# Performance work log

Hardware: AMD Instinct MI355X
Metric: run time of the kernel (lower is better)

Reference implementation:

```python
import jax, jax.numpy as jnp
import numpy as np

B, C, L = 8, 256, 2048


def setup_inputs() -> dict:
    key = jax.random.key(0)
    ks = jax.random.split(key, 7)
    s = 0.05
    return {
        "x": jax.random.normal(ks[0], (B, C, L), dtype=jnp.float32),
        "Wq": jax.random.normal(ks[1], (C, C), dtype=jnp.float32) * s,
        "bq": jax.random.normal(ks[2], (C,), dtype=jnp.float32) * s,
        "Wk": jax.random.normal(ks[3], (C, C), dtype=jnp.float32) * s,
        "bk": jax.random.normal(ks[4], (C,), dtype=jnp.float32) * s,
        "Wv": jax.random.normal(ks[5], (C, C), dtype=jnp.float32) * s,
        "bv": jax.random.normal(ks[6], (C,), dtype=jnp.float32) * s,
    }


def reference(x, Wq, bq, Wk, bk, Wv, bv):
    # Conv1d with kernel_size=1 == per-position linear over channels.
    # x: [B, C, L]
    scale = x.shape[1] ** (-0.5)
    q = jnp.einsum('oc,bcl->bol', Wq, x) + bq[None, :, None]  # [B,C,L]
    k = jnp.einsum('oc,bcl->bol', Wk, x) + bk[None, :, None]
    v = jnp.einsum('oc,bcl->bol', Wv, x) + bv[None, :, None]
    scores = jnp.einsum('bcl,bcm->blm', q, k) * scale          # [B,L,L]
    attn = jax.nn.softmax(scores, axis=-1)
    context = jnp.einsum('blm,bcm->bcl', attn, v)              # [B,C,L]
    return context + x
```

## Files before the change

### kernel.cpp

```cpp
#include <hip/hip_runtime.h>

#define NB 8
#define NC 256
#define NL 2048
#define SCALE 0.0625f

typedef __attribute__((ext_vector_type(8))) __bf16 bf16x8;
typedef __attribute__((ext_vector_type(4))) float f32x4;
typedef __attribute__((ext_vector_type(4))) unsigned int u32x4;
typedef __attribute__((ext_vector_type(2))) unsigned int u32x2;
typedef __attribute__((ext_vector_type(4))) unsigned short u16x4;
typedef __attribute__((ext_vector_type(8))) unsigned short u16x8;

static __device__ __forceinline__ unsigned short f2b(float f) {
    unsigned int u = __builtin_bit_cast(unsigned int, f);
    u += 0x7fffu + ((u >> 16) & 1u);
    return (unsigned short)(u >> 16);
}

__global__ void wconv_kernel(const float* __restrict__ Wq,
                             const float* __restrict__ Wk,
                             const float* __restrict__ Wv,
                             unsigned short* __restrict__ Wbf)
{
    const int base = (blockIdx.x * 256 + threadIdx.x) * 4;
    const int mat  = base >> 16;
    const int off  = base & 65535;
    const float* W = (mat == 0) ? Wq : (mat == 1) ? Wk : Wv;
    float4 w = *(const float4*)&W[off];
    u16x4 p = {f2b(w.x), f2b(w.y), f2b(w.z), f2b(w.w)};
    *(u16x4*)&Wbf[base] = p;
}

__global__ __launch_bounds__(256, 2) void xprep_kernel(
    const float* __restrict__ x, unsigned short* __restrict__ xT)
{
    const int b  = blockIdx.z;
    const int c0 = blockIdx.y * 64;
    const int l0 = blockIdx.x * 64;
    const int t  = threadIdx.x;

    __shared__ unsigned short Tr[64][68];

    #pragma unroll
    for (int p = 0; p < 4; ++p) {
        const int c  = p * 16 + (t >> 4);
        const int lg = t & 15;
        float4 xv = *(const float4*)&x[((size_t)(b * NC + c0 + c)) * NL + l0 + lg * 4];
        u16x4 pk = {f2b(xv.x), f2b(xv.y), f2b(xv.z), f2b(xv.w)};
        *(u16x4*)&Tr[c][lg * 4] = pk;
    }
    __syncthreads();
    #pragma unroll
    for (int j = 0; j < 2; ++j) {
        const int chunk = t + 256 * j;
        const int l  = chunk >> 3;
        const int ck = chunk & 7;
        u16x8 o;
        #pragma unroll
        for (int i = 0; i < 8; ++i) o[i] = Tr[ck * 8 + i][l];
        *(u16x8*)&xT[((size_t)(b * NL + l0 + l)) * NC + c0 + ck * 8] = o;
    }
}

__global__ __launch_bounds__(256, 2) void qkv_mfma(
    const unsigned short* __restrict__ xT,
    const unsigned short* __restrict__ Wbf,
    const float* __restrict__ bq, const float* __restrict__ bk,
    const float* __restrict__ bv,
    unsigned short* __restrict__ qT, unsigned short* __restrict__ kT,
    unsigned short* __restrict__ vo)
{
    const int raw = blockIdx.x;
    const int b   = raw & 7;
    const int rem = raw >> 3;
    const int mat = rem >> 5;
    const int lt0 = (rem & 31) * 64;
    const int t    = threadIdx.x;
    const int w    = t >> 6;
    const int lane = t & 63;
    const int ln15 = lane & 15;
    const int quad = lane >> 4;

    __shared__ __align__(16) unsigned short XT[64 * 256];
    __shared__ __align__(16) unsigned short WC[256 * 64];

    const unsigned short* Wm = Wbf + mat * 65536;
    const float* bias = (mat == 0) ? bq : (mat == 1) ? bk : bv;

    float bvals[4][4];
    #pragma unroll
    for (int ot = 0; ot < 4; ++ot)
        #pragma unroll
        for (int r = 0; r < 4; ++r)
            bvals[ot][r] = bias[w * 64 + ot * 16 + quad * 4 + r];

    #pragma unroll
    for (int s = 0; s < 8; ++s) {
        const int il = w * 8 + s;
        const int n  = il * 2 + (lane >> 5);
        const int p  = lane & 31;
        const int g  = p ^ (n & 15);
        const unsigned short* gp = &xT[((size_t)(b * NL + lt0 + n)) * NC + g * 8];
        __builtin_amdgcn_global_load_lds(
            (const __attribute__((address_space(1))) unsigned int*)gp,
            (__attribute__((address_space(3))) unsigned int*)&XT[il * 512],
            16, 0, 0);
    }

    f32x4 acc[4][4];
    #pragma unroll
    for (int i = 0; i < 4; ++i)
        #pragma unroll
        for (int j = 0; j < 4; ++j) acc[i][j] = f32x4{0.f, 0.f, 0.f, 0.f};

    for (int k0 = 0; k0 < 4; ++k0) {
        if (k0) __syncthreads();
        #pragma unroll
        for (int s = 0; s < 8; ++s) {
            const int il = w * 8 + s;
            const int o  = il * 8 + (lane >> 3);
            const int p  = lane & 7;
            const int g  = p ^ (o & 7);
            const unsigned short* gp = &Wm[(size_t)o * NC + k0 * 64 + g * 8];
            __builtin_amdgcn_global_load_lds(
                (const __attribute__((address_space(1))) unsigned int*)gp,
                (__attribute__((address_space(3))) unsigned int*)&WC[il * 512],
                16, 0, 0);
        }
        __syncthreads();

        #pragma unroll
        for (int ks = 0; ks < 2; ++ks) {
            bf16x8 xf[4];
            #pragma unroll
            for (int lt = 0; lt < 4; ++lt) {
                const int l  = lt * 16 + ln15;
                const int kc = k0 * 8 + ks * 4 + quad;
                const int pp = kc ^ (l & 15);
                xf[lt] = __builtin_bit_cast(bf16x8, *(const u32x4*)&XT[l * 256 + pp * 8]);
            }
            #pragma unroll
            for (int ot = 0; ot < 4; ++ot) {
                const int o  = w * 64 + ot * 16 + ln15;
                const int pp = (ks * 4 + quad) ^ (o & 7);
                bf16x8 wf = __builtin_bit_cast(bf16x8, *(const u32x4*)&WC[o * 64 + pp * 8]);
                #pragma unroll
                for (int lt = 0; lt < 4; ++lt)
                    acc[ot][lt] = __builtin_amdgcn_mfma_f32_16x16x32_bf16(
                                      wf, xf[lt], acc[ot][lt], 0, 0, 0);
            }
        }
    }

    if (mat < 2) {
        unsigned short* out = (mat == 0) ? qT : kT;
        #pragma unroll
        for (int ot = 0; ot < 4; ++ot) {
            const int o_base = w * 64 + ot * 16 + quad * 4;
            #pragma unroll
            for (int lt = 0; lt < 4; ++lt) {
                const int l = lt0 + lt * 16 + ln15;
                u16x4 pk;
                #pragma unroll
                for (int r = 0; r < 4; ++r)
                    pk[r] = f2b(acc[ot][lt][r] + bvals[ot][r]);
                *(u16x4*)&out[((size_t)(b * NL + l)) * NC + o_base] = pk;
            }
        }
    } else {
        #pragma unroll
        for (int ot = 0; ot < 4; ++ot)
            #pragma unroll
            for (int lt = 0; lt < 4; ++lt) {
                const int l = lt0 + lt * 16 + ln15;
                #pragma unroll
                for (int r = 0; r < 4; ++r) {
                    const int o = w * 64 + ot * 16 + quad * 4 + r;
                    vo[((size_t)(b * NC + o)) * NL + l] = f2b(acc[ot][lt][r] + bvals[ot][r]);
                }
            }
    }
}

__global__ __launch_bounds__(1024, 4) void attn_kernel(
    const unsigned short* __restrict__ qT,
    const unsigned short* __restrict__ kT,
    const unsigned short* __restrict__ v,
    const float* __restrict__ x,
    float* __restrict__ out)
{
    const int raw  = blockIdx.x;
    const int b    = raw & 7;
    const int l0   = (raw >> 3) * 64;
    const int t    = threadIdx.x;
    const int w    = t >> 6;
    const int lane = t & 63;
    const int ln15 = lane & 15;
    const int quad = lane >> 4;
    const int qg   = w & 3;
    const int kg   = w >> 2;

    __shared__ __align__(16) char smem[139264];
    unsigned short* Kb0 = (unsigned short*)smem;
    unsigned short* Kb1 = (unsigned short*)(smem + 32768);
    unsigned short* Vb0 = (unsigned short*)(smem + 65536);
    unsigned short* Vb1 = (unsigned short*)(smem + 98304);
    char* Plds = smem + 131072;
    float (*buf)[68] = (float(*)[68])smem;

    bf16x8 qf[8];
    {
        const size_t qrow = ((size_t)b * NL + l0 + qg * 16 + ln15) * NC;
        #pragma unroll
        for (int kt = 0; kt < 8; ++kt)
            qf[kt] = __builtin_bit_cast(bf16x8,
                        *(const u32x4*)&qT[qrow + kt * 32 + quad * 8]);
    }

    f32x4 ctx[4];
    #pragma unroll
    for (int i = 0; i < 4; ++i) ctx[i] = f32x4{0.f, 0.f, 0.f, 0.f};
    f32x4 dacc = f32x4{0.f, 0.f, 0.f, 0.f};

    const u16x8 ones_u = {0x3F80, 0x3F80, 0x3F80, 0x3F80,
                          0x3F80, 0x3F80, 0x3F80, 0x3F80};
    const bf16x8 onesf = __builtin_bit_cast(bf16x8, ones_u);

    auto stage = [&](int mt, unsigned short* Kd, unsigned short* Vd) {
        const int m0 = mt * 64;
        #pragma unroll
        for (int s = 0; s < 2; ++s) {
            const int il = w * 2 + s;
            const int n  = il * 2 + (lane >> 5);
            const int g  = (lane & 31) ^ (n & 15);
            const unsigned short* gp = &kT[((size_t)b * NL + m0 + n) * NC + g * 8];
            __builtin_amdgcn_global_load_lds(
                (const __attribute__((address_space(1))) unsigned int*)gp,
                (__attribute__((address_space(3))) unsigned int*)&Kd[il * 512],
                16, 0, 0);
        }
        #pragma unroll
        for (int s = 0; s < 2; ++s) {
            const int il = w * 2 + s;
            const int c  = il * 8 + (lane >> 3);
            const int g  = (lane & 7) ^ (c & 7);
            const unsigned short* gp = &v[((size_t)(b * NC + c)) * NL + m0 + g * 8];
            __builtin_amdgcn_global_load_lds(
                (const __attribute__((address_space(1))) unsigned int*)gp,
                (__attribute__((address_space(3))) unsigned int*)&Vd[il * 512],
                16, 0, 0);
        }
    };

    stage(0, Kb0, Vb0);
    __syncthreads();

    const int q    = qg * 16 + ln15;
    const int pwof = q * 128 + (((kg * 32) + quad * 8) ^ ((q & 7) << 4));
    int prof[2];
    #pragma unroll
    for (int jw = 0; jw < 2; ++jw)
        prof[jw] = q * 128 + ((jw * 64 + quad * 16) ^ ((q & 7) << 4));

    for (int mt = 0; mt < 32; ++mt) {
        if (mt < 31) {
            if (mt & 1) stage(mt + 1, Kb0, Vb0);
            else        stage(mt + 1, Kb1, Vb1);
        }
        const unsigned short* Kd = (mt & 1) ? Kb1 : Kb0;
        const unsigned short* Vd = (mt & 1) ? Vb1 : Vb0;

        f32x4 sacc = f32x4{0.f, 0.f, 0.f, 0.f};
        {
            const int n = kg * 16 + ln15;
            #pragma unroll
            for (int kt = 0; kt < 8; ++kt) {
                const int p = (kt * 4 + quad) ^ (n & 15);
                bf16x8 kf = __builtin_bit_cast(bf16x8,
                              *(const u32x4*)&Kd[n * 256 + p * 8]);
                sacc = __builtin_amdgcn_mfma_f32_16x16x32_bf16(
                           kf, qf[kt], sacc, 0, 0, 0);
            }
        }

        {
            float e0 = __expf(sacc[0] * SCALE);
            float e1 = __expf(sacc[1] * SCALE);
            float e2 = __expf(sacc[2] * SCALE);
            float e3 = __expf(sacc[3] * SCALE);
            unsigned int d0 = (unsigned int)f2b(e0) | ((unsigned int)f2b(e1) << 16);
            unsigned int d1 = (unsigned int)f2b(e2) | ((unsigned int)f2b(e3) << 16);
            *(u32x2*)(Plds + pwof) = u32x2{d0, d1};
        }

        asm volatile("s_waitcnt lgkmcnt(0)" ::: "memory");
        __builtin_amdgcn_s_barrier();
        __builtin_amdgcn_sched_barrier(0);

        bf16x8 pa[2];
        #pragma unroll
        for (int jw = 0; jw < 2; ++jw)
            pa[jw] = __builtin_bit_cast(bf16x8, *(const u32x4*)(Plds + prof[jw]));

        dacc = __builtin_amdgcn_mfma_f32_16x16x32_bf16(pa[0], onesf, dacc, 0, 0, 0);
        dacc = __builtin_amdgcn_mfma_f32_16x16x32_bf16(pa[1], onesf, dacc, 0, 0, 0);

        #pragma unroll
        for (int ct = 0; ct < 4; ++ct) {
            const int c = kg * 64 + ct * 16 + ln15;
            #pragma unroll
            for (int jw = 0; jw < 2; ++jw) {
                const int p = (jw * 4 + quad) ^ (c & 7);
                bf16x8 vb = __builtin_bit_cast(bf16x8,
                              *(const u32x4*)&Vd[c * 64 + p * 8]);
                ctx[ct] = __builtin_amdgcn_mfma_f32_16x16x32_bf16(
                              pa[jw], vb, ctx[ct], 0, 0, 0);
            }
        }

        __syncthreads();
    }

    {
        float rinv[4];
        #pragma unroll
        for (int r = 0; r < 4; ++r) rinv[r] = 1.0f / dacc[r];
        #pragma unroll
        for (int ct = 0; ct < 4; ++ct) {
            const int c = kg * 64 + ct * 16 + ln15;
            #pragma unroll
            for (int r = 0; r < 4; ++r)
                buf[c][qg * 16 + quad * 4 + r] = ctx[ct][r] * rinv[r];
        }
    }
    __syncthreads();

    #pragma unroll
    for (int p = 0; p < 4; ++p) {
        const int f  = t + 1024 * p;
        const int c  = f >> 4;
        const int lg = (f & 15) * 4;
        const size_t idx = ((size_t)(b * NC + c)) * NL + l0 + lg;
        float4 xv = *(const float4*)&x[idx];
        float4 cv = *(const float4*)&buf[c][lg];
        float4 o = make_float4(cv.x + xv.x, cv.y + xv.y, cv.z + xv.z, cv.w + xv.w);
        *(float4*)&out[idx] = o;
    }
}

extern "C" void kernel_launch(void* const* d_in, const int* in_sizes, int n_in,
                              void* d_out, int out_size, void* d_ws, size_t ws_size,
                              hipStream_t stream) {
    const float* x  = (const float*)d_in[0];
    const float* Wq = (const float*)d_in[1];
    const float* bq = (const float*)d_in[2];
    const float* Wk = (const float*)d_in[3];
    const float* bk = (const float*)d_in[4];
    const float* Wv = (const float*)d_in[5];
    const float* bv = (const float*)d_in[6];
    float* out = (float*)d_out;

    const size_t plane = (size_t)NB * NC * NL;
    unsigned short* qT  = (unsigned short*)d_ws;
    unsigned short* kT  = qT + plane;
    unsigned short* v   = kT + plane;
    unsigned short* xT  = v + plane;
    unsigned short* Wbf = xT + plane;

    wconv_kernel<<<192, 256, 0, stream>>>(Wq, Wk, Wv, Wbf);

    dim3 gx(NL / 64, NC / 64, NB);
    xprep_kernel<<<gx, 256, 0, stream>>>(x, xT);

    qkv_mfma<<<768, 256, 0, stream>>>(xT, Wbf, bq, bk, bv, qT, kT, v);

    attn_kernel<<<256, 1024, 0, stream>>>(qT, kT, v, x, out);
}
```

Before: 154.1 us.

## Load K and V fragments directly from global memory instead of LDS staging

Removes the double-buffered global-to-LDS staging of K and V tiles. Each wave now reads its MFMA operands straight from global memory into registers every iteration. This cuts LDS usage roughly in half and removes the LDS round trip. In exchange, waves that share K/V rows load them redundantly, and global load latency is no longer overlapped with compute by prefetch.

```diff
diff --git a/kernel.cpp b/kernel.cpp
--- a/kernel.cpp
+++ b/kernel.cpp
@@ -201,12 +201,8 @@
     const int qg   = w & 3;
     const int kg   = w >> 2;
 
-    __shared__ __align__(16) char smem[139264];
-    unsigned short* Kb0 = (unsigned short*)smem;
-    unsigned short* Kb1 = (unsigned short*)(smem + 32768);
-    unsigned short* Vb0 = (unsigned short*)(smem + 65536);
-    unsigned short* Vb1 = (unsigned short*)(smem + 98304);
-    char* Plds = smem + 131072;
+    __shared__ __align__(16) char smem[69632];
+    char* Plds = smem;
     float (*buf)[68] = (float(*)[68])smem;
 
     bf16x8 qf[8];
@@ -227,35 +223,6 @@
                           0x3F80, 0x3F80, 0x3F80, 0x3F80};
     const bf16x8 onesf = __builtin_bit_cast(bf16x8, ones_u);
 
-    auto stage = [&](int mt, unsigned short* Kd, unsigned short* Vd) {
-        const int m0 = mt * 64;
-        #pragma unroll
-        for (int s = 0; s < 2; ++s) {
-            const int il = w * 2 + s;
-            const int n  = il * 2 + (lane >> 5);
-            const int g  = (lane & 31) ^ (n & 15);
-            const unsigned short* gp = &kT[((size_t)b * NL + m0 + n) * NC + g * 8];
-            __builtin_amdgcn_global_load_lds(
-                (const __attribute__((address_space(1))) unsigned int*)gp,
-                (__attribute__((address_space(3))) unsigned int*)&Kd[il * 512],
-                16, 0, 0);
-        }
-        #pragma unroll
-        for (int s = 0; s < 2; ++s) {
-            const int il = w * 2 + s;
-            const int c  = il * 8 + (lane >> 3);
-            const int g  = (lane & 7) ^ (c & 7);
-            const unsigned short* gp = &v[((size_t)(b * NC + c)) * NL + m0 + g * 8];
-            __builtin_amdgcn_global_load_lds(
-                (const __attribute__((address_space(1))) unsigned int*)gp,
-                (__attribute__((address_space(3))) unsigned int*)&Vd[il * 512],
-                16, 0, 0);
-        }
-    };
-
-    stage(0, Kb0, Vb0);
-    __syncthreads();
-
     const int q    = qg * 16 + ln15;
     const int pwof = q * 128 + (((kg * 32) + quad * 8) ^ ((q & 7) << 4));
     int prof[2];
@@ -263,26 +230,22 @@
     for (int jw = 0; jw < 2; ++jw)
         prof[jw] = q * 128 + ((jw * 64 + quad * 16) ^ ((q & 7) << 4));
 
+    const unsigned short* kbase =
+        kT + ((size_t)b * NL + kg * 16 + ln15) * NC + quad * 8;
+
     for (int mt = 0; mt < 32; ++mt) {
-        if (mt < 31) {
-            if (mt & 1) stage(mt + 1, Kb0, Vb0);
-            else        stage(mt + 1, Kb1, Vb1);
-        }
-        const unsigned short* Kd = (mt & 1) ? Kb1 : Kb0;
-        const unsigned short* Vd = (mt & 1) ? Vb1 : Vb0;
-
+        const size_t mof = (size_t)mt * 64 * NC;
+
+        bf16x8 kf[8];
+        #pragma unroll
+        for (int kt = 0; kt < 8; ++kt)
+            kf[kt] = __builtin_bit_cast(bf16x8,
+                        *(const u32x4*)(kbase + mof + kt * 32));
         f32x4 sacc = f32x4{0.f, 0.f, 0.f, 0.f};
-        {
-            const int n = kg * 16 + ln15;
-            #pragma unroll
-            for (int kt = 0; kt < 8; ++kt) {
-                const int p = (kt * 4 + quad) ^ (n & 15);
-                bf16x8 kf = __builtin_bit_cast(bf16x8,
-                              *(const u32x4*)&Kd[n * 256 + p * 8]);
-                sacc = __builtin_amdgcn_mfma_f32_16x16x32_bf16(
-                           kf, qf[kt], sacc, 0, 0, 0);
-            }
-        }
+        #pragma unroll
+        for (int kt = 0; kt < 8; ++kt)
+            sacc = __builtin_amdgcn_mfma_f32_16x16x32_bf16(
+                       kf[kt], qf[kt], sacc, 0, 0, 0);
 
         {
             float e0 = __expf(sacc[0] * SCALE);
@@ -303,20 +266,25 @@
         for (int jw = 0; jw < 2; ++jw)
             pa[jw] = __builtin_bit_cast(bf16x8, *(const u32x4*)(Plds + prof[jw]));
 
+        bf16x8 vb[4][2];
+        #pragma unroll
+        for (int ct = 0; ct < 4; ++ct) {
+            const int c = kg * 64 + ct * 16 + ln15;
+            const unsigned short* vrow =
+                v + ((size_t)(b * NC + c)) * NL + mt * 64 + quad * 8;
+            vb[ct][0] = __builtin_bit_cast(bf16x8, *(const u32x4*)vrow);
+            vb[ct][1] = __builtin_bit_cast(bf16x8, *(const u32x4*)(vrow + 32));
+        }
+
         dacc = __builtin_amdgcn_mfma_f32_16x16x32_bf16(pa[0], onesf, dacc, 0, 0, 0);
         dacc = __builtin_amdgcn_mfma_f32_16x16x32_bf16(pa[1], onesf, dacc, 0, 0, 0);
 
         #pragma unroll
         for (int ct = 0; ct < 4; ++ct) {
-            const int c = kg * 64 + ct * 16 + ln15;
-            #pragma unroll
-            for (int jw = 0; jw < 2; ++jw) {
-                const int p = (jw * 4 + quad) ^ (c & 7);
-                bf16x8 vb = __builtin_bit_cast(bf16x8,
-                              *(const u32x4*)&Vd[c * 64 + p * 8]);
-                ctx[ct] = __builtin_amdgcn_mfma_f32_16x16x32_bf16(
-                              pa[jw], vb, ctx[ct], 0, 0, 0);
-            }
+            ctx[ct] = __builtin_amdgcn_mfma_f32_16x16x32_bf16(
+                          pa[0], vb[ct][0], ctx[ct], 0, 0, 0);
+            ctx[ct] = __builtin_amdgcn_mfma_f32_16x16x32_bf16(
+                          pa[1], vb[ct][1], ctx[ct], 0, 0, 0);
         }
 
         __syncthreads();
```

New measurement: 340.4 us. 121% more time.

## Software-pipeline QK^T and PV stages across iterations with double-buffered P

Applied to the files above, without the earlier changes.

Restructures the attention loop so that iteration mt computes the QK^T scores and exp for tile mt while running the PV MFMAs for tile mt-1, using double-buffered P tiles in LDS. This removes the mid-iteration barrier. K and V staging are split so V for tile mt is loaded one iteration later than K. The QK^T accumulation is also split into two independent accumulators to shorten the MFMA dependency chain. LDS use grows by 8 KB and the loop gains one extra drain iteration.

```diff
diff --git a/kernel.cpp b/kernel.cpp
--- a/kernel.cpp
+++ b/kernel.cpp
@@ -201,12 +201,13 @@
     const int qg   = w & 3;
     const int kg   = w >> 2;
 
-    __shared__ __align__(16) char smem[139264];
+    __shared__ __align__(16) char smem[147456];
     unsigned short* Kb0 = (unsigned short*)smem;
-    unsigned short* Kb1 = (unsigned short*)(smem + 32768);
-    unsigned short* Vb0 = (unsigned short*)(smem + 65536);
+    unsigned short* Vb0 = (unsigned short*)(smem + 32768);
+    unsigned short* Kb1 = (unsigned short*)(smem + 65536);
     unsigned short* Vb1 = (unsigned short*)(smem + 98304);
-    char* Plds = smem + 131072;
+    char* P0 = smem + 131072;
+    char* P1 = smem + 139264;
     float (*buf)[68] = (float(*)[68])smem;
 
     bf16x8 qf[8];
@@ -227,7 +228,7 @@
                           0x3F80, 0x3F80, 0x3F80, 0x3F80};
     const bf16x8 onesf = __builtin_bit_cast(bf16x8, ones_u);
 
-    auto stage = [&](int mt, unsigned short* Kd, unsigned short* Vd) {
+    auto stageK = [&](int mt, unsigned short* Kd) {
         const int m0 = mt * 64;
         #pragma unroll
         for (int s = 0; s < 2; ++s) {
@@ -240,6 +241,9 @@
                 (__attribute__((address_space(3))) unsigned int*)&Kd[il * 512],
                 16, 0, 0);
         }
+    };
+    auto stageV = [&](int mt, unsigned short* Vd) {
+        const int m0 = mt * 64;
         #pragma unroll
         for (int s = 0; s < 2; ++s) {
             const int il = w * 2 + s;
@@ -253,9 +257,6 @@
         }
     };
 
-    stage(0, Kb0, Vb0);
-    __syncthreads();
-
     const int q    = qg * 16 + ln15;
     const int pwof = q * 128 + (((kg * 32) + quad * 8) ^ ((q & 7) << 4));
     int prof[2];
@@ -263,60 +264,65 @@
     for (int jw = 0; jw < 2; ++jw)
         prof[jw] = q * 128 + ((jw * 64 + quad * 16) ^ ((q & 7) << 4));
 
-    for (int mt = 0; mt < 32; ++mt) {
-        if (mt < 31) {
-            if (mt & 1) stage(mt + 1, Kb0, Vb0);
-            else        stage(mt + 1, Kb1, Vb1);
-        }
-        const unsigned short* Kd = (mt & 1) ? Kb1 : Kb0;
-        const unsigned short* Vd = (mt & 1) ? Vb1 : Vb0;
-
-        f32x4 sacc = f32x4{0.f, 0.f, 0.f, 0.f};
-        {
+    stageK(0, Kb0);
+    __syncthreads();
+
+    for (int mt = 0; mt <= 32; ++mt) {
+        if (mt < 31) stageK(mt + 1, (mt & 1) ? Kb0 : Kb1);
+        if (mt < 32) stageV(mt, (mt & 1) ? Vb1 : Vb0);
+
+        f32x4 sacc0 = f32x4{0.f, 0.f, 0.f, 0.f};
+        f32x4 sacc1 = f32x4{0.f, 0.f, 0.f, 0.f};
+        if (mt < 32) {
+            const unsigned short* Kd = (mt & 1) ? Kb1 : Kb0;
             const int n = kg * 16 + ln15;
             #pragma unroll
-            for (int kt = 0; kt < 8; ++kt) {
-                const int p = (kt * 4 + quad) ^ (n & 15);
-                bf16x8 kf = __builtin_bit_cast(bf16x8,
-                              *(const u32x4*)&Kd[n * 256 + p * 8]);
-                sacc = __builtin_amdgcn_mfma_f32_16x16x32_bf16(
-                           kf, qf[kt], sacc, 0, 0, 0);
-            }
-        }
-
-        {
-            float e0 = __expf(sacc[0] * SCALE);
-            float e1 = __expf(sacc[1] * SCALE);
-            float e2 = __expf(sacc[2] * SCALE);
-            float e3 = __expf(sacc[3] * SCALE);
+            for (int kt = 0; kt < 8; kt += 2) {
+                const int p0 = (kt * 4 + quad) ^ (n & 15);
+                const int p1 = ((kt + 1) * 4 + quad) ^ (n & 15);
+                bf16x8 kf0 = __builtin_bit_cast(bf16x8,
+                               *(const u32x4*)&Kd[n * 256 + p0 * 8]);
+                bf16x8 kf1 = __builtin_bit_cast(bf16x8,
+                               *(const u32x4*)&Kd[n * 256 + p1 * 8]);
+                sacc0 = __builtin_amdgcn_mfma_f32_16x16x32_bf16(
+                            kf0, qf[kt], sacc0, 0, 0, 0);
+                sacc1 = __builtin_amdgcn_mfma_f32_16x16x32_bf16(
+                            kf1, qf[kt + 1], sacc1, 0, 0, 0);
+            }
+        }
+
+        if (mt > 0) {
+            const char* Pr = ((mt - 1) & 1) ? P1 : P0;
+            const unsigned short* Vd = ((mt - 1) & 1) ? Vb1 : Vb0;
+            bf16x8 pa[2];
+            #pragma unroll
+            for (int jw = 0; jw < 2; ++jw)
+                pa[jw] = __builtin_bit_cast(bf16x8, *(const u32x4*)(Pr + prof[jw]));
+            dacc = __builtin_amdgcn_mfma_f32_16x16x32_bf16(pa[0], onesf, dacc, 0, 0, 0);
+            dacc = __builtin_amdgcn_mfma_f32_16x16x32_bf16(pa[1], onesf, dacc, 0, 0, 0);
+            #pragma unroll
+            for (int ct = 0; ct < 4; ++ct) {
+                const int c = kg * 64 + ct * 16 + ln15;
+                #pragma unroll
+                for (int jw = 0; jw < 2; ++jw) {
+                    const int p = (jw * 4 + quad) ^ (c & 7);
+                    bf16x8 vb = __builtin_bit_cast(bf16x8,
+                                  *(const u32x4*)&Vd[c * 64 + p * 8]);
+                    ctx[ct] = __builtin_amdgcn_mfma_f32_16x16x32_bf16(
+                                  pa[jw], vb, ctx[ct], 0, 0, 0);
+                }
+            }
+        }
+
+        if (mt < 32) {
+            char* Pw = (mt & 1) ? P1 : P0;
+            float e0 = __expf((sacc0[0] + sacc1[0]) * SCALE);
+            float e1 = __expf((sacc0[1] + sacc1[1]) * SCALE);
+            float e2 = __expf((sacc0[2] + sacc1[2]) * SCALE);
+            float e3 = __expf((sacc0[3] + sacc1[3]) * SCALE);
             unsigned int d0 = (unsigned int)f2b(e0) | ((unsigned int)f2b(e1) << 16);
             unsigned int d1 = (unsigned int)f2b(e2) | ((unsigned int)f2b(e3) << 16);
-            *(u32x2*)(Plds + pwof) = u32x2{d0, d1};
-        }
-
-        asm volatile("s_waitcnt lgkmcnt(0)" ::: "memory");
-        __builtin_amdgcn_s_barrier();
-        __builtin_amdgcn_sched_barrier(0);
-
-        bf16x8 pa[2];
-        #pragma unroll
-        for (int jw = 0; jw < 2; ++jw)
-            pa[jw] = __builtin_bit_cast(bf16x8, *(const u32x4*)(Plds + prof[jw]));
-
-        dacc = __builtin_amdgcn_mfma_f32_16x16x32_bf16(pa[0], onesf, dacc, 0, 0, 0);
-        dacc = __builtin_amdgcn_mfma_f32_16x16x32_bf16(pa[1], onesf, dacc, 0, 0, 0);
-
-        #pragma unroll
-        for (int ct = 0; ct < 4; ++ct) {
-            const int c = kg * 64 + ct * 16 + ln15;
-            #pragma unroll
-            for (int jw = 0; jw < 2; ++jw) {
-                const int p = (jw * 4 + quad) ^ (c & 7);
-                bf16x8 vb = __builtin_bit_cast(bf16x8,
-                              *(const u32x4*)&Vd[c * 64 + p * 8]);
-                ctx[ct] = __builtin_amdgcn_mfma_f32_16x16x32_bf16(
-                              pa[jw], vb, ctx[ct], 0, 0, 0);
-            }
+            *(u32x2*)(Pw + pwof) = u32x2{d0, d1};
         }
 
         __syncthreads();
```

Result: no change. 153.6 us (-0.4%).

## Split waves into QK/softmax and PV producer-consumer groups with skewed pipeline

Applied to the files above, without the earlier changes.

Waves are split into two roles. Eight waves compute QK^T scores and exponentials for tile r and write P into a double-buffered LDS slot. The other eight waves run the P·V MFMAs for tile r-1, which overlaps exp and softmax work with the PV matmul. The row-sum denominator now comes from shuffle reductions and a final LDS reduction, replacing the ones-vector MFMA. The cost is more LDS, an extra loop iteration, and each wave carrying two query sub-tiles, which raises register pressure under launch_bounds(1024,4).

```diff
diff --git a/kernel.cpp b/kernel.cpp
--- a/kernel.cpp
+++ b/kernel.cpp
@@ -198,36 +198,42 @@
     const int lane = t & 63;
     const int ln15 = lane & 15;
     const int quad = lane >> 4;
-    const int qg   = w & 3;
-    const int kg   = w >> 2;
-
-    __shared__ __align__(16) char smem[139264];
+    const bool isQK = (w < 8);
+    const int kg  = w & 3;
+    const int qh  = isQK ? (w >> 2) : ((w - 8) >> 2);
+    const int ch  = (w - 8) & 3;
+
+    __shared__ __align__(16) char smem[148480];
     unsigned short* Kb0 = (unsigned short*)smem;
     unsigned short* Kb1 = (unsigned short*)(smem + 32768);
     unsigned short* Vb0 = (unsigned short*)(smem + 65536);
     unsigned short* Vb1 = (unsigned short*)(smem + 98304);
-    char* Plds = smem + 131072;
+    char* P0 = smem + 131072;
+    char* P1 = smem + 139264;
+    float* denomLDS = (float*)(smem + 147456);
     float (*buf)[68] = (float(*)[68])smem;
 
-    bf16x8 qf[8];
-    {
-        const size_t qrow = ((size_t)b * NL + l0 + qg * 16 + ln15) * NC;
-        #pragma unroll
-        for (int kt = 0; kt < 8; ++kt)
-            qf[kt] = __builtin_bit_cast(bf16x8,
-                        *(const u32x4*)&qT[qrow + kt * 32 + quad * 8]);
-    }
-
-    f32x4 ctx[4];
-    #pragma unroll
-    for (int i = 0; i < 4; ++i) ctx[i] = f32x4{0.f, 0.f, 0.f, 0.f};
-    f32x4 dacc = f32x4{0.f, 0.f, 0.f, 0.f};
-
-    const u16x8 ones_u = {0x3F80, 0x3F80, 0x3F80, 0x3F80,
-                          0x3F80, 0x3F80, 0x3F80, 0x3F80};
-    const bf16x8 onesf = __builtin_bit_cast(bf16x8, ones_u);
-
-    auto stage = [&](int mt, unsigned short* Kd, unsigned short* Vd) {
+    bf16x8 qf0[8], qf1[8];
+    if (isQK) {
+        const size_t qrow0 = ((size_t)b * NL + l0 + qh * 32 + ln15) * NC;
+        const size_t qrow1 = qrow0 + (size_t)16 * NC;
+        #pragma unroll
+        for (int kt = 0; kt < 8; ++kt) {
+            qf0[kt] = __builtin_bit_cast(bf16x8,
+                         *(const u32x4*)&qT[qrow0 + kt * 32 + quad * 8]);
+            qf1[kt] = __builtin_bit_cast(bf16x8,
+                         *(const u32x4*)&qT[qrow1 + kt * 32 + quad * 8]);
+        }
+    }
+
+    f32x4 ctx[2][4];
+    #pragma unroll
+    for (int i = 0; i < 2; ++i)
+        #pragma unroll
+        for (int j = 0; j < 4; ++j) ctx[i][j] = f32x4{0.f, 0.f, 0.f, 0.f};
+    float dacc0 = 0.f, dacc1 = 0.f;
+
+    auto stageK = [&](int mt, unsigned short* Kd) {
         const int m0 = mt * 64;
         #pragma unroll
         for (int s = 0; s < 2; ++s) {
@@ -240,6 +246,9 @@
                 (__attribute__((address_space(3))) unsigned int*)&Kd[il * 512],
                 16, 0, 0);
         }
+    };
+    auto stageV = [&](int mt, unsigned short* Vd) {
+        const int m0 = mt * 64;
         #pragma unroll
         for (int s = 0; s < 2; ++s) {
             const int il = w * 2 + s;
@@ -253,85 +262,106 @@
         }
     };
 
-    stage(0, Kb0, Vb0);
+    stageK(0, Kb0);
     __syncthreads();
 
-    const int q    = qg * 16 + ln15;
-    const int pwof = q * 128 + (((kg * 32) + quad * 8) ^ ((q & 7) << 4));
-    int prof[2];
-    #pragma unroll
-    for (int jw = 0; jw < 2; ++jw)
-        prof[jw] = q * 128 + ((jw * 64 + quad * 16) ^ ((q & 7) << 4));
-
-    for (int mt = 0; mt < 32; ++mt) {
-        if (mt < 31) {
-            if (mt & 1) stage(mt + 1, Kb0, Vb0);
-            else        stage(mt + 1, Kb1, Vb1);
-        }
-        const unsigned short* Kd = (mt & 1) ? Kb1 : Kb0;
-        const unsigned short* Vd = (mt & 1) ? Vb1 : Vb0;
-
-        f32x4 sacc = f32x4{0.f, 0.f, 0.f, 0.f};
-        {
-            const int n = kg * 16 + ln15;
-            #pragma unroll
-            for (int kt = 0; kt < 8; ++kt) {
-                const int p = (kt * 4 + quad) ^ (n & 15);
-                bf16x8 kf = __builtin_bit_cast(bf16x8,
-                              *(const u32x4*)&Kd[n * 256 + p * 8]);
-                sacc = __builtin_amdgcn_mfma_f32_16x16x32_bf16(
-                           kf, qf[kt], sacc, 0, 0, 0);
-            }
-        }
-
-        {
-            float e0 = __expf(sacc[0] * SCALE);
-            float e1 = __expf(sacc[1] * SCALE);
-            float e2 = __expf(sacc[2] * SCALE);
-            float e3 = __expf(sacc[3] * SCALE);
-            unsigned int d0 = (unsigned int)f2b(e0) | ((unsigned int)f2b(e1) << 16);
-            unsigned int d1 = (unsigned int)f2b(e2) | ((unsigned int)f2b(e3) << 16);
-            *(u32x2*)(Plds + pwof) = u32x2{d0, d1};
-        }
-
-        asm volatile("s_waitcnt lgkmcnt(0)" ::: "memory");
-        __builtin_amdgcn_s_barrier();
-        __builtin_amdgcn_sched_barrier(0);
-
-        bf16x8 pa[2];
-        #pragma unroll
-        for (int jw = 0; jw < 2; ++jw)
-            pa[jw] = __builtin_bit_cast(bf16x8, *(const u32x4*)(Plds + prof[jw]));
-
-        dacc = __builtin_amdgcn_mfma_f32_16x16x32_bf16(pa[0], onesf, dacc, 0, 0, 0);
-        dacc = __builtin_amdgcn_mfma_f32_16x16x32_bf16(pa[1], onesf, dacc, 0, 0, 0);
-
-        #pragma unroll
-        for (int ct = 0; ct < 4; ++ct) {
-            const int c = kg * 64 + ct * 16 + ln15;
-            #pragma unroll
-            for (int jw = 0; jw < 2; ++jw) {
-                const int p = (jw * 4 + quad) ^ (c & 7);
-                bf16x8 vb = __builtin_bit_cast(bf16x8,
-                              *(const u32x4*)&Vd[c * 64 + p * 8]);
-                ctx[ct] = __builtin_amdgcn_mfma_f32_16x16x32_bf16(
-                              pa[jw], vb, ctx[ct], 0, 0, 0);
+    for (int r = 0; r <= 32; ++r) {
+        if (r < 31) stageK(r + 1, ((r + 1) & 1) ? Kb1 : Kb0);
+        if (r < 32) stageV(r, (r & 1) ? Vb1 : Vb0);
+
+        if (isQK) {
+            if (r < 32) {
+                const unsigned short* Kd = (r & 1) ? Kb1 : Kb0;
+                const int n = kg * 16 + ln15;
+                f32x4 s0 = f32x4{0.f, 0.f, 0.f, 0.f};
+                f32x4 s1 = f32x4{0.f, 0.f, 0.f, 0.f};
+                #pragma unroll
+                for (int kt = 0; kt < 8; ++kt) {
+                    const int p = (kt * 4 + quad) ^ (n & 15);
+                    bf16x8 kf = __builtin_bit_cast(bf16x8,
+                                  *(const u32x4*)&Kd[n * 256 + p * 8]);
+                    s0 = __builtin_amdgcn_mfma_f32_16x16x32_bf16(kf, qf0[kt], s0, 0, 0, 0);
+                    s1 = __builtin_amdgcn_mfma_f32_16x16x32_bf16(kf, qf1[kt], s1, 0, 0, 0);
+                }
+                char* Pw = (r & 1) ? P1 : P0;
+                const int q0 = qh * 32 + ln15;
+                const int q1 = q0 + 16;
+                const int wo = (kg * 32 + quad * 8) ^ ((q0 & 7) << 4);
+                float e00 = __expf(s0[0] * SCALE), e01 = __expf(s0[1] * SCALE);
+                float e02 = __expf(s0[2] * SCALE), e03 = __expf(s0[3] * SCALE);
+                float e10 = __expf(s1[0] * SCALE), e11 = __expf(s1[1] * SCALE);
+                float e12 = __expf(s1[2] * SCALE), e13 = __expf(s1[3] * SCALE);
+                unsigned int d0 = (unsigned int)f2b(e00) | ((unsigned int)f2b(e01) << 16);
+                unsigned int d1 = (unsigned int)f2b(e02) | ((unsigned int)f2b(e03) << 16);
+                unsigned int d2 = (unsigned int)f2b(e10) | ((unsigned int)f2b(e11) << 16);
+                unsigned int d3 = (unsigned int)f2b(e12) | ((unsigned int)f2b(e13) << 16);
+                *(u32x2*)(Pw + q0 * 128 + wo) = u32x2{d0, d1};
+                *(u32x2*)(Pw + q1 * 128 + wo) = u32x2{d2, d3};
+                float rs0 = (e00 + e01) + (e02 + e03);
+                float rs1 = (e10 + e11) + (e12 + e13);
+                rs0 += __shfl_xor(rs0, 16, 64);
+                rs0 += __shfl_xor(rs0, 32, 64);
+                rs1 += __shfl_xor(rs1, 16, 64);
+                rs1 += __shfl_xor(rs1, 32, 64);
+                dacc0 += rs0;
+                dacc1 += rs1;
+            }
+        } else {
+            if (r > 0) {
+                const char* Pr = ((r - 1) & 1) ? P1 : P0;
+                const unsigned short* Vd = ((r - 1) & 1) ? Vb1 : Vb0;
+                bf16x8 pa[2][2];
+                #pragma unroll
+                for (int row = 0; row < 2; ++row) {
+                    const int qr = qh * 32 + row * 16 + ln15;
+                    #pragma unroll
+                    for (int jw = 0; jw < 2; ++jw)
+                        pa[row][jw] = __builtin_bit_cast(bf16x8,
+                            *(const u32x4*)(Pr + qr * 128 +
+                                ((jw * 64 + quad * 16) ^ ((qr & 7) << 4))));
+                }
+                #pragma unroll
+                for (int ct = 0; ct < 4; ++ct) {
+                    const int c = ch * 64 + ct * 16 + ln15;
+                    #pragma unroll
+                    for (int jw = 0; jw < 2; ++jw) {
+                        const int p = (jw * 4 + quad) ^ (c & 7);
+                        bf16x8 vb = __builtin_bit_cast(bf16x8,
+                                      *(const u32x4*)&Vd[c * 64 + p * 8]);
+                        ctx[0][ct] = __builtin_amdgcn_mfma_f32_16x16x32_bf16(
+                                         pa[0][jw], vb, ctx[0][ct], 0, 0, 0);
+                        ctx[1][ct] = __builtin_amdgcn_mfma_f32_16x16x32_bf16(
+                                         pa[1][jw], vb, ctx[1][ct], 0, 0, 0);
+                    }
+                }
             }
         }
 
         __syncthreads();
     }
 
-    {
-        float rinv[4];
-        #pragma unroll
-        for (int r = 0; r < 4; ++r) rinv[r] = 1.0f / dacc[r];
-        #pragma unroll
-        for (int ct = 0; ct < 4; ++ct) {
-            const int c = kg * 64 + ct * 16 + ln15;
-            #pragma unroll
-            for (int r = 0; r < 4; ++r)
-                buf[c][qg * 16 + quad * 4 + r] = ctx[ct][r] * rinv[r];
+    if (isQK && quad == 0) {
+        denomLDS[kg * 64 + qh * 32 + ln15]      = dacc0;
+        denomLDS[kg * 64 + qh * 32 + 16 + ln15] = dacc1;
+    }
+    __syncthreads();
+    if (!isQK) {
+        #pragma unroll
+        for (int row = 0; row < 2; ++row) {
+            float rinv[4];
+            #pragma unroll
+            for (int rr = 0; rr < 4; ++rr) {
+                const int q = qh * 32 + row * 16 + quad * 4 + rr;
+                rinv[rr] = 1.0f / (denomLDS[q] + denomLDS[64 + q] +
+                                   denomLDS[128 + q] + denomLDS[192 + q]);
+            }
+            #pragma unroll
+            for (int ct = 0; ct < 4; ++ct) {
+                const int c = ch * 64 + ct * 16 + ln15;
+                #pragma unroll
+                for (int rr = 0; rr < 4; ++rr)
+                    buf[c][qh * 32 + row * 16 + quad * 4 + rr] = ctx[row][ct][rr] * rinv[rr];
+            }
         }
     }
     __syncthreads();
```

New measurement: 190.6 us. +23.7%, slower.
